# Kernel tuning notes

Hardware: AMD Instinct MI355X
Metric: run time of the kernel (lower is better)

## Reference

```python
import jax, jax.numpy as jnp
import numpy as np

B, T, A, IN = 128, 512, 2, 192
N_SESS, RDIM, OUT = 512, 64, 256


def setup_inputs() -> dict:
    key = jax.random.key(0)
    k1, k2, k3, k4 = jax.random.split(key, 4)
    state_in = jax.random.normal(k1, (B, T, A, IN), dtype=jnp.float32)
    session = jax.random.randint(k2, (B,), 0, N_SESS, dtype=jnp.int64)
    # kaiming-uniform-like init scale, exact distribution irrelevant for correctness baseline
    unique_readin = jax.random.normal(k3, (N_SESS, IN, RDIM), dtype=jnp.float32) * (1.0 / np.sqrt(IN))
    project = jax.random.normal(k4, (RDIM, OUT), dtype=jnp.float32) * (1.0 / np.sqrt(RDIM))
    return {"state_in": state_in, "session": session,
            "unique_readin": unique_readin, "project": project}


def reference(state_in, session, unique_readin, project):
    # gather per-sample readin matrices: [B, IN, RDIM]
    readin_matrix = unique_readin[session]
    # btai,bih->btah : per-sample matmul over the input-feature axis
    h = jnp.einsum('btai,bih->btah', state_in, readin_matrix)
    # low-rank compression projection to model dim: [B, T, A, OUT]
    out = jnp.matmul(h, project)
    return out
```

## Files before the change

kernel.cpp:

```cpp
#include <hip/hip_runtime.h>
#include <hip/hip_bf16.h>
#include <stdint.h>


typedef short    bf16x8 __attribute__((ext_vector_type(8)));
typedef float    f32x4  __attribute__((ext_vector_type(4)));
typedef uint32_t u32x4  __attribute__((ext_vector_type(4)));

#define NB    128
#define MPB   1024
#define INF   192
#define RDIM  64
#define OUTF  256

#define WAIT_VM6() asm volatile("s_waitcnt vmcnt(6)" ::: "memory")
#define WAIT_VM0() asm volatile("s_waitcnt vmcnt(0)" ::: "memory")

__device__ __forceinline__ uint16_t f2bf(float f) {
    union { float f; uint32_t u; } v; v.f = f;
    return (uint16_t)((v.u + 0x7fffu + ((v.u >> 16) & 1u)) >> 16);
}
__device__ __forceinline__ uint32_t pack2(float a, float b) {
    return (uint32_t)f2bf(a) | ((uint32_t)f2bf(b) << 16);
}

__device__ __forceinline__ bf16x8 cvt8(f32x4 a, f32x4 b) {
    union { __hip_bfloat162 h2[4]; bf16x8 h; } r;
    r.h2[0] = __float22bfloat162_rn({a[0], a[1]});
    r.h2[1] = __float22bfloat162_rn({a[2], a[3]});
    r.h2[2] = __float22bfloat162_rn({b[0], b[1]});
    r.h2[3] = __float22bfloat162_rn({b[2], b[3]});
    return r.h;
}

__device__ __forceinline__ void gl_lds16(const void* g, void* l) {
    auto gp = (const __attribute__((address_space(1))) uint32_t*)(uintptr_t)g;
    auto lp = (__attribute__((address_space(3))) uint32_t*)(uintptr_t)l;
    __builtin_amdgcn_global_load_lds(gp, lp, 16, 0, 0);
}

__global__ __launch_bounds__(256) void k1_build_w(
    const float* __restrict__ readin,
    const float* __restrict__ project,
    const int*   __restrict__ session,
    uint16_t*    __restrict__ Wt)
{
    __shared__ uint16_t Rl[INF * 64];
    __shared__ uint16_t Pl[128 * 64];

    const int b  = blockIdx.x >> 1;
    const int oh = blockIdx.x & 1;
    const int t  = threadIdx.x;
    const float* Rg = readin + (size_t)session[b] * (INF * RDIM);

#pragma unroll
    for (int c = 0; c < 3; ++c) {
        int idx = c * 4096 + t * 16;
        int row = idx >> 6;
        int kg0 = (idx & 63) >> 3;
        f32x4 v0 = *(const f32x4*)(Rg + idx);
        f32x4 v1 = *(const f32x4*)(Rg + idx + 4);
        f32x4 v2 = *(const f32x4*)(Rg + idx + 8);
        f32x4 v3 = *(const f32x4*)(Rg + idx + 12);
        u32x4 d0, d1;
        d0[0] = pack2(v0[0], v0[1]); d0[1] = pack2(v0[2], v0[3]);
        d0[2] = pack2(v1[0], v1[1]); d0[3] = pack2(v1[2], v1[3]);
        d1[0] = pack2(v2[0], v2[1]); d1[1] = pack2(v2[2], v2[3]);
        d1[2] = pack2(v3[0], v3[1]); d1[3] = pack2(v3[2], v3[3]);
        *(u32x4*)&Rl[row * 64 + (((kg0    ) ^ (row & 7)) << 3)] = d0;
        *(u32x4*)&Rl[row * 64 + (((kg0 + 1) ^ (row & 7)) << 3)] = d1;
    }
    {
        int h  = t >> 2;
        int og = (t & 3) * 32;
        const float* Pg = project + (size_t)h * OUTF + oh * 128 + og;
#pragma unroll
        for (int q = 0; q < 8; ++q) {
            f32x4 v = *(const f32x4*)(Pg + q * 4);
#pragma unroll
            for (int e = 0; e < 4; ++e) {
                int o = og + q * 4 + e;
                Pl[o * 64 + (((h >> 3) ^ (o & 7)) << 3) + (h & 7)] = f2bf(v[e]);
            }
        }
    }
    __syncthreads();

    const int l  = t & 63, w = t >> 6;
    const int wm = w >> 1, wn = w & 1;
    const int lr = l & 15, lk = l >> 4;

    f32x4 acc[4][6];
#pragma unroll
    for (int m = 0; m < 4; ++m)
#pragma unroll
        for (int n = 0; n < 6; ++n) acc[m][n] = f32x4{0.f, 0.f, 0.f, 0.f};

#pragma unroll
    for (int kk = 0; kk < 2; ++kk) {
        int kg = kk * 4 + lk;
        bf16x8 a[4], bb[6];
#pragma unroll
        for (int m = 0; m < 4; ++m) {
            int row = wm * 64 + m * 16 + lr;
            a[m] = *(const bf16x8*)&Pl[row * 64 + ((kg ^ (row & 7)) << 3)];
        }
#pragma unroll
        for (int n = 0; n < 6; ++n) {
            int col = wn * 96 + n * 16 + lr;
            bb[n] = *(const bf16x8*)&Rl[col * 64 + ((kg ^ (col & 7)) << 3)];
        }
#pragma unroll
        for (int m = 0; m < 4; ++m)
#pragma unroll
            for (int n = 0; n < 6; ++n)
                acc[m][n] = __builtin_amdgcn_mfma_f32_16x16x32_bf16(
                    a[m], bb[n], acc[m][n], 0, 0, 0);
    }

    uint16_t* Wb = Wt + ((size_t)b * OUTF + oh * 128) * INF;
#pragma unroll
    for (int m = 0; m < 4; ++m) {
        int o = wm * 64 + m * 16 + lk * 4;
#pragma unroll
        for (int n = 0; n < 6; ++n) {
            int i = wn * 96 + n * 16 + lr;
#pragma unroll
            for (int j = 0; j < 4; ++j)
                Wb[(size_t)(o + j) * INF + i] = f2bf(acc[m][n][j]);
        }
    }
}

__global__ __launch_bounds__(256, 2) void k2_gemm(
    const float*    __restrict__ X,
    const uint16_t* __restrict__ Wt,
    float*          __restrict__ Y)
{
    __shared__ uint8_t  As[3][16384];
    __shared__ uint16_t Bs[3][4096];

    const int bid0 = blockIdx.x;
    const int bid  = ((bid0 & 7) << 8) | (bid0 >> 3);
    const int b  = bid >> 4;
    const int mt = (bid >> 1) & 7;
    const int nt = bid & 1;
    const int t  = threadIdx.x, l = t & 63, w = t >> 6;

    const float*    Xb = X  + ((size_t)b * MPB  + mt * 128) * INF;
    const uint16_t* Wb = Wt + ((size_t)b * OUTF + nt * 128) * INF;
    float*          Yb = Y  + ((size_t)b * MPB  + mt * 128) * OUTF + nt * 128;

    int aoff[4];
#pragma unroll
    for (int j = 0; j < 4; ++j) {
        int c = w * 4 + j;
        aoff[j] = (c * 8 + (l >> 3)) * INF + (((l & 7) ^ (l >> 3)) << 2);
    }
    int boff[2];
#pragma unroll
    for (int j = 0; j < 2; ++j) {
        int c = w * 2 + j;
        boff[j] = (c * 16 + (l >> 2)) * INF + (((l & 3) ^ ((l >> 2) & 3)) << 3);
    }

    auto stage = [&](int ks, int buf) {
#pragma unroll
        for (int j = 0; j < 4; ++j)
            gl_lds16(Xb + aoff[j] + ks * 32, &As[buf][(w * 4 + j) * 1024]);
#pragma unroll
        for (int j = 0; j < 2; ++j)
            gl_lds16(Wb + boff[j] + ks * 32, &Bs[buf][(w * 2 + j) * 512]);
    };

    stage(0, 0);
    stage(1, 1);

    const int wm = w >> 1, wn = w & 1;
    const int lr = l & 15, lk = l >> 4;
    const int as0 = (((2 * lk)     ^ (lr & 7)) << 4);
    const int as1 = (((2 * lk + 1) ^ (lr & 7)) << 4);
    const int bs0 = ((lk ^ (lr & 3)) << 4);

    f32x4 acc[4][4];
#pragma unroll
    for (int m = 0; m < 4; ++m)
#pragma unroll
        for (int n = 0; n < 4; ++n) acc[m][n] = f32x4{0.f, 0.f, 0.f, 0.f};

#pragma unroll
    for (int ks = 0; ks < 6; ++ks) {
        const int cur = ks % 3;
        if (ks < 5) { WAIT_VM6(); } else { WAIT_VM0(); }
        __builtin_amdgcn_s_barrier();
        __builtin_amdgcn_sched_barrier(0);
        if (ks < 4) stage(ks + 2, (ks + 2) % 3);

        bf16x8 af[4], bfr[4];
#pragma unroll
        for (int m = 0; m < 4; ++m) {
            int row = wm * 64 + m * 16 + lr;
            const uint8_t* p = &As[cur][row * 128];
            f32x4 lo = *(const f32x4*)(p + as0);
            f32x4 hi = *(const f32x4*)(p + as1);
            af[m] = cvt8(lo, hi);
        }
#pragma unroll
        for (int n = 0; n < 4; ++n) {
            int rn = wn * 64 + n * 16 + lr;
            bfr[n] = *(const bf16x8*)((const uint8_t*)&Bs[cur][0] + rn * 64 + bs0);
        }
#pragma unroll
        for (int m = 0; m < 4; ++m)
#pragma unroll
            for (int n = 0; n < 4; ++n)
                acc[m][n] = __builtin_amdgcn_mfma_f32_16x16x32_bf16(
                    af[m], bfr[n], acc[m][n], 0, 0, 0);
    }

#pragma unroll
    for (int m = 0; m < 4; ++m) {
        int r0 = wm * 64 + m * 16 + lk * 4;
#pragma unroll
        for (int n = 0; n < 4; ++n) {
            int c0 = wn * 64 + n * 16 + lr;
#pragma unroll
            for (int j = 0; j < 4; ++j)
                Yb[(size_t)(r0 + j) * OUTF + c0] = acc[m][n][j];
        }
    }
}

extern "C" void kernel_launch(void* const* d_in, const int* in_sizes, int n_in,
                              void* d_out, int out_size, void* d_ws, size_t ws_size,
                              hipStream_t stream) {
    (void)in_sizes; (void)n_in; (void)out_size; (void)ws_size;
    const float* state   = (const float*)d_in[0];
    const int*   session = (const int*)  d_in[1];
    const float* readin  = (const float*)d_in[2];
    const float* project = (const float*)d_in[3];
    float*    out = (float*)d_out;
    uint16_t* Wt  = (uint16_t*)d_ws;

    hipLaunchKernelGGL(k1_build_w, dim3(256), dim3(256), 0, stream,
                       readin, project, session, Wt);
    hipLaunchKernelGGL(k2_gemm, dim3(2048), dim3(256), 0, stream,
                       state, Wt, out);
}
```

Baseline: 54.04 us.

## Convert X tile to bf16 in registers before LDS, shrink LDS for occupancy

The A operand (fp32 activations) was previously copied into LDS as fp32 via direct global-to-LDS loads and converted to bf16 on every fragment read. It is now loaded into registers, converted once, and written to LDS as bf16 in a k-slot-major layout, which halves the A tile's LDS footprint. B uses the same k-slot-major layout, so fragment reads become plain 16-byte loads. With less LDS per block, launch bounds go to 3 blocks per CU. The cost is more registers for the prefetched fp32 data, an extra LDS write plus lgkmcnt wait in each iteration, and possible bank conflicts from the unswizzled layout.

New measurement: 61.28 us. 1.13x slower.

```diff
diff --git a/kernel.cpp b/kernel.cpp
--- a/kernel.cpp
+++ b/kernel.cpp
@@ -15,6 +15,7 @@
 
 #define WAIT_VM6() asm volatile("s_waitcnt vmcnt(6)" ::: "memory")
 #define WAIT_VM0() asm volatile("s_waitcnt vmcnt(0)" ::: "memory")
+#define WAIT_LGKM0() asm volatile("s_waitcnt lgkmcnt(0)" ::: "memory")
 
 __device__ __forceinline__ uint16_t f2bf(float f) {
     union { float f; uint32_t u; } v; v.f = f;
@@ -132,13 +133,13 @@
     }
 }
 
-__global__ __launch_bounds__(256, 2) void k2_gemm(
+__global__ __launch_bounds__(256, 3) void k2_gemm(
     const float*    __restrict__ X,
     const uint16_t* __restrict__ Wt,
     float*          __restrict__ Y)
 {
-    __shared__ uint8_t  As[3][16384];
-    __shared__ uint16_t Bs[3][4096];
+    __shared__ uint8_t As[3][8192];
+    __shared__ uint8_t Bs[3][8192];
 
     const int bid0 = blockIdx.x;
     const int bid  = ((bid0 & 7) << 8) | (bid0 >> 3);
@@ -151,36 +152,48 @@
     const uint16_t* Wb = Wt + ((size_t)b * OUTF + nt * 128) * INF;
     float*          Yb = Y  + ((size_t)b * MPB  + mt * 128) * OUTF + nt * 128;
 
-    int aoff[4];
-#pragma unroll
-    for (int j = 0; j < 4; ++j) {
-        int c = w * 4 + j;
-        aoff[j] = (c * 8 + (l >> 3)) * INF + (((l & 7) ^ (l >> 3)) << 2);
-    }
-    int boff[2];
+    const int ar  = t >> 1;
+    const int akh = t & 1;
+    const float* asrc = Xb + (size_t)ar * INF + akh * 16;
+    const int aw0 = (akh * 2    ) * 2048 + ar * 16;
+    const int aw1 = (akh * 2 + 1) * 2048 + ar * 16;
+
+    int boff[2], bchunk[2];
 #pragma unroll
     for (int j = 0; j < 2; ++j) {
-        int c = w * 2 + j;
-        boff[j] = (c * 16 + (l >> 2)) * INF + (((l & 3) ^ ((l >> 2) & 3)) << 3);
-    }
-
-    auto stage = [&](int ks, int buf) {
-#pragma unroll
-        for (int j = 0; j < 4; ++j)
-            gl_lds16(Xb + aoff[j] + ks * 32, &As[buf][(w * 4 + j) * 1024]);
+        int c  = w * 2 + j;
+        int i  = c * 64 + l;
+        int kslot = i >> 7;
+        int n  = i & 127;
+        boff[j]   = n * INF + kslot * 8;
+        bchunk[j] = c;
+    }
+
+    f32x4 pa0[4], pa1[4];
+
+    auto issueA = [&](int ks, f32x4* pa) {
+        const float* p = asrc + ks * 32;
+        pa[0] = *(const f32x4*)(p);
+        pa[1] = *(const f32x4*)(p + 4);
+        pa[2] = *(const f32x4*)(p + 8);
+        pa[3] = *(const f32x4*)(p + 12);
+    };
+    auto issueB = [&](int ks, int buf) {
 #pragma unroll
         for (int j = 0; j < 2; ++j)
-            gl_lds16(Wb + boff[j] + ks * 32, &Bs[buf][(w * 2 + j) * 512]);
+            gl_lds16(Wb + boff[j] + ks * 32, &Bs[buf][bchunk[j] * 1024]);
     };
-
-    stage(0, 0);
-    stage(1, 1);
+    auto writeA = [&](int buf, const f32x4* pa) {
+        *(bf16x8*)&As[buf][aw0] = cvt8(pa[0], pa[1]);
+        *(bf16x8*)&As[buf][aw1] = cvt8(pa[2], pa[3]);
+    };
+
+    issueA(0, pa0); issueB(0, 0);
+    issueA(1, pa1); issueB(1, 1);
 
     const int wm = w >> 1, wn = w & 1;
     const int lr = l & 15, lk = l >> 4;
-    const int as0 = (((2 * lk)     ^ (lr & 7)) << 4);
-    const int as1 = (((2 * lk + 1) ^ (lr & 7)) << 4);
-    const int bs0 = ((lk ^ (lr & 3)) << 4);
+    const int fofs = lk * 2048 + lr * 16;
 
     f32x4 acc[4][4];
 #pragma unroll
@@ -192,24 +205,24 @@
     for (int ks = 0; ks < 6; ++ks) {
         const int cur = ks % 3;
         if (ks < 5) { WAIT_VM6(); } else { WAIT_VM0(); }
+        __builtin_amdgcn_sched_barrier(0);
+        writeA(cur, (ks & 1) ? pa1 : pa0);
+        WAIT_LGKM0();
         __builtin_amdgcn_s_barrier();
         __builtin_amdgcn_sched_barrier(0);
-        if (ks < 4) stage(ks + 2, (ks + 2) % 3);
+        if (ks < 4) {
+            issueA(ks + 2, (ks & 1) ? pa1 : pa0);
+            issueB(ks + 2, (ks + 2) % 3);
+        }
+        __builtin_amdgcn_sched_barrier(0);
 
         bf16x8 af[4], bfr[4];
 #pragma unroll
-        for (int m = 0; m < 4; ++m) {
-            int row = wm * 64 + m * 16 + lr;
-            const uint8_t* p = &As[cur][row * 128];
-            f32x4 lo = *(const f32x4*)(p + as0);
-            f32x4 hi = *(const f32x4*)(p + as1);
-            af[m] = cvt8(lo, hi);
-        }
-#pragma unroll
-        for (int n = 0; n < 4; ++n) {
-            int rn = wn * 64 + n * 16 + lr;
-            bfr[n] = *(const bf16x8*)((const uint8_t*)&Bs[cur][0] + rn * 64 + bs0);
-        }
+        for (int m = 0; m < 4; ++m)
+            af[m] = *(const bf16x8*)&As[cur][fofs + (wm * 64 + m * 16) * 16];
+#pragma unroll
+        for (int n = 0; n < 4; ++n)
+            bfr[n] = *(const bf16x8*)&Bs[cur][fofs + (wn * 64 + n * 16) * 16];
 #pragma unroll
         for (int m = 0; m < 4; ++m)
 #pragma unroll
```
